# Optimization experiments

Hardware: AMD Instinct MI355X
Metric: run time of the kernel (lower is better)

## Reference

```python
import jax, jax.numpy as jnp
import numpy as np

EPS = 1e-12  # F.normalize eps


def _l2norm(v, axis):
    n = jnp.sqrt(jnp.sum(v * v, axis=axis, keepdims=True))
    return v / jnp.maximum(n, EPS)


def setup_inputs() -> dict:
    key = jax.random.key(0)
    k1, k2, k3, k4 = jax.random.split(key, 4)
    N, C, H, W = 48, 512, 40, 40
    K = 64
    x = jax.random.normal(k1, (N, C, H, W), dtype=jnp.float32)
    conv_w = jax.random.normal(k2, (K, C), dtype=jnp.float32) * 0.02   # cluster-assign 1x1 conv, no bias (vladv2=False)
    attn_w = jax.random.normal(k3, (1, C), dtype=jnp.float32) * 0.02   # heatmap 1x1 conv
    attn_b = jnp.zeros((1,), dtype=jnp.float32)
    centroids = jax.random.uniform(k4, (K, C), dtype=jnp.float32)      # torch.rand init
    return {"x": x, "conv_w": conv_w, "attn_w": attn_w, "attn_b": attn_b, "centroids": centroids}


def reference(x, conv_w, attn_w, attn_b, centroids):
    N, C, H, W = x.shape
    K = conv_w.shape[0]
    P = H * W

    # attention heatmap: ReLU -> 1x1 conv -> ReLU  => [N, 1, H, W]
    hmp = jax.nn.relu(jnp.einsum('nchw,oc->nohw', jax.nn.relu(x), attn_w) + attn_b[None, :, None, None])
    hmp_flat = hmp.reshape(N, 1, P)  # [N,1,P]

    # normalize input descriptors across channels
    xn = _l2norm(x, axis=1)                      # [N,C,H,W]
    x_flat = xn.reshape(N, C, P)                 # [N,C,P]

    # soft assignment: 1x1 conv over clusters + softmax over cluster dim
    logits = jnp.einsum('ncp,kc->nkp', x_flat, conv_w)   # [N,K,P]
    soft_assign = jax.nn.softmax(logits, axis=1)          # softmax over K

    # weighted residual aggregation, fused:
    # vlad[n,k,c] = sum_p (x[n,c,p] - centroids[k,c]) * sa[n,k,p] * hmp[n,0,p]
    w = soft_assign * hmp_flat                            # [N,K,P]
    term1 = jnp.einsum('nkp,ncp->nkc', w, x_flat)         # [N,K,C]
    wsum = jnp.sum(w, axis=-1)                            # [N,K]
    vlad = term1 - wsum[:, :, None] * centroids[None, :, :]

    vlad = _l2norm(vlad, axis=2)                          # intra-normalize per cluster
    vlad = vlad.reshape(N, K * C)
    vlad = _l2norm(vlad, axis=1)                          # global L2 normalize
    return vlad
```

## Files before the change

kernel.cpp:

```cpp
#include <hip/hip_runtime.h>
#include <math.h>

#define NN 48
#define CC 512
#define KK 64
#define PP 1600
#define EPSF 1e-12f

typedef short short8 __attribute__((ext_vector_type(8)));
typedef float f32x4 __attribute__((ext_vector_type(4)));

static __device__ __forceinline__ unsigned short f2bf(float f) {
    unsigned u = __float_as_uint(f);
    u += 0x7fffu + ((u >> 16) & 1u);
    return (unsigned short)(u >> 16);
}
static __device__ __forceinline__ unsigned pack2(float a, float b) {
    return (unsigned)f2bf(a) | ((unsigned)f2bf(b) << 16);
}

static __device__ __forceinline__ void barrier_nd() {
    asm volatile("s_waitcnt lgkmcnt(0)\n\ts_barrier" ::: "memory");
}

__global__ __launch_bounds__(256, 4) void kn_logits(
    const float* __restrict__ x, const float* __restrict__ conv_w,
    const float* __restrict__ attn_w, const float* __restrict__ attn_b,
    unsigned short* __restrict__ wg, float* __restrict__ wsum,
    unsigned short* __restrict__ xbf)
{
    __shared__ unsigned short xt[64][76];
    __shared__ unsigned short cwb[64][72];
    __shared__ float attn_l[CC];
    __shared__ float red[16][64];
    __shared__ float invn_l[64];
    __shared__ float hmp_l[64];
    __shared__ float wsum_l[KK];

    const int n = blockIdx.y, p0 = blockIdx.x * 64, tid = threadIdx.x;
    const int q = tid & 15, cg = tid >> 4;
    const int wave = tid >> 6, lane = tid & 63;
    const int lq = lane >> 4, lm = lane & 15;
    const int kr = tid >> 2, cq = tid & 3;

    for (int i = tid; i < CC; i += 256) attn_l[i] = attn_w[i];
    if (tid < KK) wsum_l[tid] = 0.f;

    f32x4 acc[4];
#pragma unroll
    for (int mt = 0; mt < 4; ++mt) acc[mt] = (f32x4){0.f, 0.f, 0.f, 0.f};
    float ss[4] = {0.f, 0.f, 0.f, 0.f};
    float ad[4] = {0.f, 0.f, 0.f, 0.f};

    const float* xb = x + (size_t)n * CC * PP;
    const float* wp0 = conv_w + (size_t)kr * CC + cq * 16;
    const float* xp0 = xb + (size_t)(cg * 4) * PP + p0 + 4 * q;

    float4 wv[4], xv[4];
#pragma unroll
    for (int j = 0; j < 4; ++j) wv[j] = *(const float4*)(wp0 + 4 * j);
#pragma unroll
    for (int j = 0; j < 4; ++j) xv[j] = *(const float4*)(xp0 + (size_t)j * PP);

    __syncthreads();

#pragma unroll 1
    for (int cs = 0; cs < 8; ++cs) {
        float4 wn[4], xn_[4];
        if (cs < 7) {
            const float* wp = wp0 + (cs + 1) * 64;
            const float* xp = xp0 + (size_t)(cs + 1) * 64 * PP;
#pragma unroll
            for (int j = 0; j < 4; ++j) wn[j] = *(const float4*)(wp + 4 * j);
#pragma unroll
            for (int j = 0; j < 4; ++j) xn_[j] = *(const float4*)(xp + (size_t)j * PP);
        }
#pragma unroll
        for (int j = 0; j < 4; ++j) {
            uint2 u = {pack2(wv[j].x, wv[j].y), pack2(wv[j].z, wv[j].w)};
            *(uint2*)&cwb[kr][cq * 16 + 4 * j] = u;
        }
        const int cbase = cs * 64 + cg * 4;
#pragma unroll
        for (int j = 0; j < 4; ++j) {
            float4 v = xv[j];
            const float aw = attn_l[cbase + j];
            ss[0] += v.x * v.x; ss[1] += v.y * v.y;
            ss[2] += v.z * v.z; ss[3] += v.w * v.w;
            ad[0] += fmaxf(v.x, 0.f) * aw; ad[1] += fmaxf(v.y, 0.f) * aw;
            ad[2] += fmaxf(v.z, 0.f) * aw; ad[3] += fmaxf(v.w, 0.f) * aw;
            uint2 u = {pack2(v.x, v.y), pack2(v.z, v.w)};
            *(uint2*)&xt[cg * 4 + j][4 * q] = u;
            if (xbf)
                *(uint2*)(xbf + ((size_t)n * CC + cbase + j) * PP + p0 + 4 * q) = u;
        }
        barrier_nd();
#pragma unroll
        for (int ks = 0; ks < 2; ++ks) {
            short8 af[4];
#pragma unroll
            for (int mt = 0; mt < 4; ++mt)
                af[mt] = *(const short8*)&cwb[mt * 16 + lm][ks * 32 + lq * 8];
            const int pl = wave * 16 + lm;
            const int cb = ks * 32 + lq * 8;
            short8 bv;
#pragma unroll
            for (int j = 0; j < 8; ++j) bv[j] = (short)xt[cb + j][pl];
#pragma unroll
            for (int mt = 0; mt < 4; ++mt)
                acc[mt] = __builtin_amdgcn_mfma_f32_16x16x32_bf16(
                    af[mt], bv, acc[mt], 0, 0, 0);
        }
        barrier_nd();
        if (cs < 7) {
#pragma unroll
            for (int j = 0; j < 4; ++j) { wv[j] = wn[j]; xv[j] = xn_[j]; }
        }
    }

#pragma unroll
    for (int j = 0; j < 4; ++j) red[cg][4 * q + j] = ss[j];
    __syncthreads();
    if (tid < 64) {
        float S = 0.f;
#pragma unroll
        for (int l = 0; l < 16; ++l) S += red[l][tid];
        invn_l[tid] = 1.f / fmaxf(sqrtf(S), EPSF);
    }
    __syncthreads();
#pragma unroll
    for (int j = 0; j < 4; ++j) red[cg][4 * q + j] = ad[j];
    __syncthreads();
    if (tid < 64) {
        float A = 0.f;
#pragma unroll
        for (int l = 0; l < 16; ++l) A += red[l][tid];
        hmp_l[tid] = fmaxf(A + attn_b[0], 0.f);
    }
    __syncthreads();

    const int pl = wave * 16 + lm;
    const float inv = invn_l[pl];
    const float hp = hmp_l[pl];
    float mx = -1e30f;
#pragma unroll
    for (int mt = 0; mt < 4; ++mt)
#pragma unroll
        for (int r = 0; r < 4; ++r) {
            const float l = acc[mt][r] * inv;
            acc[mt][r] = l;
            mx = fmaxf(mx, l);
        }
    mx = fmaxf(mx, __shfl_xor(mx, 16));
    mx = fmaxf(mx, __shfl_xor(mx, 32));
    float s = 0.f;
#pragma unroll
    for (int mt = 0; mt < 4; ++mt)
#pragma unroll
        for (int r = 0; r < 4; ++r) {
            const float e = __expf(acc[mt][r] - mx);
            acc[mt][r] = e;
            s += e;
        }
    s += __shfl_xor(s, 16);
    s += __shfl_xor(s, 32);
    const float sden = hp / s;

    unsigned short* wrb = wg + (size_t)n * KK * PP + p0;
#pragma unroll
    for (int mt = 0; mt < 4; ++mt)
#pragma unroll
        for (int r = 0; r < 4; ++r) {
            const int k = mt * 16 + lq * 4 + r;
            const float w0 = acc[mt][r] * sden;
            float wk = w0;
#pragma unroll
            for (int o = 1; o < 16; o <<= 1) wk += __shfl_xor(wk, o);
            if (lm == 0) atomicAdd(&wsum_l[k], wk);
            wrb[(size_t)k * PP + pl] = f2bf(w0 * inv);
        }
    __syncthreads();
    if (tid < KK) atomicAdd(&wsum[n * KK + tid], wsum_l[tid]);
}

template <bool XB>
__global__ __launch_bounds__(256) void kn_term1(
    const float* __restrict__ xf, const unsigned short* __restrict__ xbf,
    const unsigned short* __restrict__ wgq, float* __restrict__ term1p)
{
    __shared__ unsigned short wt[64][40];
    __shared__ unsigned short xt2[64][40];
    const int c0 = blockIdx.x * 64, n = blockIdx.y, ph = blockIdx.z;
    const int tid = threadIdx.x;
    const int wave = tid >> 6, lane = tid & 63, lq = lane >> 4, lm = lane & 15;
    const int koff = (wave >> 1) * 32, coff = (wave & 1) * 32;
    const int s_begin = (50 * ph) >> 2, s_end = (50 * (ph + 1)) >> 2;
    const int rA = tid >> 2, cq = tid & 3;

    f32x4 acc[2][2];
#pragma unroll
    for (int mt = 0; mt < 2; ++mt)
#pragma unroll
        for (int nt = 0; nt < 2; ++nt) acc[mt][nt] = (f32x4){0.f, 0.f, 0.f, 0.f};

    const unsigned short* wb = wgq + (size_t)n * KK * PP + (size_t)rA * PP + cq * 8;
    const unsigned short* xbb = xbf + ((size_t)n * CC + c0 + rA) * PP + cq * 8;
    const float* xfb = xf + ((size_t)n * CC + c0 + rA) * PP + cq * 8;

    auto ldB = [&](int p) -> uint4 {
        if (XB) {
            return *(const uint4*)(xbb + p);
        } else {
            const float* sp = xfb + p;
            float4 a = *(const float4*)sp, b = *(const float4*)(sp + 4);
            return make_uint4(pack2(a.x, a.y), pack2(a.z, a.w),
                              pack2(b.x, b.y), pack2(b.z, b.w));
        }
    };

    uint4 pa = *(const uint4*)(wb + s_begin * 32);
    uint4 pb = ldB(s_begin * 32);

    for (int ps = s_begin; ps < s_end; ++ps) {
        uint4 na, nb;
        if (ps + 1 < s_end) {
            na = *(const uint4*)(wb + (ps + 1) * 32);
            nb = ldB((ps + 1) * 32);
        }
        *(uint4*)&wt[rA][cq * 8] = pa;
        *(uint4*)&xt2[rA][cq * 8] = pb;
        barrier_nd();
        short8 af[2], bv[2];
#pragma unroll
        for (int mt = 0; mt < 2; ++mt)
            af[mt] = *(const short8*)&wt[koff + mt * 16 + lm][lq * 8];
#pragma unroll
        for (int nt = 0; nt < 2; ++nt)
            bv[nt] = *(const short8*)&xt2[coff + nt * 16 + lm][lq * 8];
#pragma unroll
        for (int mt = 0; mt < 2; ++mt)
#pragma unroll
            for (int nt = 0; nt < 2; ++nt)
                acc[mt][nt] = __builtin_amdgcn_mfma_f32_16x16x32_bf16(
                    af[mt], bv[nt], acc[mt][nt], 0, 0, 0);
        barrier_nd();
        pa = na; pb = nb;
    }

    float* ob = term1p + ((size_t)ph * NN + n) * KK * CC + c0 + coff;
#pragma unroll
    for (int mt = 0; mt < 2; ++mt)
#pragma unroll
        for (int r = 0; r < 4; ++r) {
            const int k = koff + mt * 16 + lq * 4 + r;
#pragma unroll
            for (int nt = 0; nt < 2; ++nt)
                ob[(size_t)k * CC + nt * 16 + lm] = acc[mt][nt][r];
        }
}

__global__ __launch_bounds__(128) void kn_vlad(
    const float* __restrict__ term1p, const float* __restrict__ wsum,
    const float* __restrict__ cent, float* __restrict__ out,
    float* __restrict__ nsum)
{
    const int k = blockIdx.x, n = blockIdx.y, tid = threadIdx.x;
    const size_t base = ((size_t)n * KK + k) * CC;
    const size_t NKC = (size_t)NN * KK * CC;
    const float ws = wsum[n * KK + k];
    const int c = tid * 4;

    float4 ce = *(const float4*)(cent + (size_t)k * CC + c);
    float4 v = {-ws * ce.x, -ws * ce.y, -ws * ce.z, -ws * ce.w};
#pragma unroll
    for (int h = 0; h < 4; ++h) {
        float4 a = *(const float4*)(term1p + h * NKC + base + c);
        v.x += a.x; v.y += a.y; v.z += a.z; v.w += a.w;
    }

    float s = v.x * v.x + v.y * v.y + v.z * v.z + v.w * v.w;
#pragma unroll
    for (int o = 32; o >= 1; o >>= 1) s += __shfl_down(s, o, 64);

    __shared__ float rb[2];
    __shared__ float sinv;
    if ((tid & 63) == 0) rb[tid >> 6] = s;
    __syncthreads();
    if (tid == 0) {
        const float S = rb[0] + rb[1];
        const float inv = 1.f / fmaxf(sqrtf(S), EPSF);
        sinv = inv;
        atomicAdd(&nsum[n], S * inv * inv);
    }
    __syncthreads();
    const float inv = sinv;
    float4 o4 = {v.x * inv, v.y * inv, v.z * inv, v.w * inv};
    *(float4*)(out + base + c) = o4;
}

__global__ __launch_bounds__(256) void kn_scale(
    float* __restrict__ out, const float* __restrict__ nsum)
{
    const int n = blockIdx.y;
    const size_t off = ((size_t)blockIdx.x * 256 + threadIdx.x) * 4;
    const float g = 1.f / fmaxf(sqrtf(nsum[n]), EPSF);
    float4 v = *(float4*)(out + (size_t)n * KK * CC + off);
    v.x *= g; v.y *= g; v.z *= g; v.w *= g;
    *(float4*)(out + (size_t)n * KK * CC + off) = v;
}

extern "C" void kernel_launch(void* const* d_in, const int* in_sizes, int n_in,
                              void* d_out, int out_size, void* d_ws, size_t ws_size,
                              hipStream_t stream)
{
    (void)in_sizes; (void)n_in; (void)out_size;
    const float* x      = (const float*)d_in[0];
    const float* conv_w = (const float*)d_in[1];
    const float* attn_w = (const float*)d_in[2];
    const float* attn_b = (const float*)d_in[3];
    const float* cent   = (const float*)d_in[4];
    float* out = (float*)d_out;

    char* w = (char*)d_ws;
    float* term1p = (float*)w;            w += (size_t)4 * NN * KK * CC * 4;
    float* wsum   = (float*)w;            w += (size_t)NN * KK * 4;
    float* nsum   = (float*)w;            w += 256;
    unsigned short* wg  = (unsigned short*)w; w += (size_t)NN * KK * PP * 2;
    unsigned short* xbf = (unsigned short*)w;
    const size_t need_xb = (size_t)(w - (char*)d_ws) + (size_t)NN * CC * PP * 2;
    const bool xb = ws_size >= need_xb;

    hipMemsetAsync(wsum, 0, NN * KK * sizeof(float), stream);
    hipMemsetAsync(nsum, 0, NN * sizeof(float), stream);

    kn_logits<<<dim3(25, NN), 256, 0, stream>>>(x, conv_w, attn_w, attn_b,
                                                wg, wsum, xb ? xbf : nullptr);
    if (xb)
        kn_term1<true><<<dim3(8, NN, 4), 256, 0, stream>>>(x, xbf, wg, term1p);
    else
        kn_term1<false><<<dim3(8, NN, 4), 256, 0, stream>>>(x, xbf, wg, term1p);
    kn_vlad <<<dim3(KK, NN), 128, 0, stream>>>(term1p, wsum, cent, out, nsum);
    kn_scale<<<dim3(32, NN), 256, 0, stream>>>(out, nsum);
}
```

Baseline: 324.1 us.

## Use direct global-to-LDS DMA with double buffering in logits and term1 kernels

Both the logits and term1 kernels now load input tiles with global_load_lds straight into double-buffered, XOR-swizzled shared memory. The next chunk's copy is issued before the current one is computed. Register staging goes away and the bf16 conversion in logits now happens on read from LDS. The aim is to hide global memory latency and cut VGPR pressure. In exchange, the fp32 tile doubles LDS use, the occupancy hint drops from 4 to 3 blocks, and correctness now depends on hand-written vmcnt waits.

```diff
diff --git a/kernel.cpp b/kernel.cpp
--- a/kernel.cpp
+++ b/kernel.cpp
@@ -23,19 +23,21 @@
     asm volatile("s_waitcnt lgkmcnt(0)\n\ts_barrier" ::: "memory");
 }
 
-__global__ __launch_bounds__(256, 4) void kn_logits(
+typedef __attribute__((address_space(3))) unsigned int as3_uint;
+typedef __attribute__((address_space(1))) const unsigned int as1_cuint;
+static __device__ __forceinline__ void dma16(const void* g, void* l) {
+    __builtin_amdgcn_global_load_lds((as1_cuint*)g, (as3_uint*)l, 16, 0, 0);
+}
+
+__global__ __launch_bounds__(256, 3) void kn_logits(
     const float* __restrict__ x, const float* __restrict__ conv_w,
     const float* __restrict__ attn_w, const float* __restrict__ attn_b,
     unsigned short* __restrict__ wg, float* __restrict__ wsum,
     unsigned short* __restrict__ xbf)
 {
-    __shared__ unsigned short xt[64][76];
+    __shared__ float xf[2][64][64];
     __shared__ unsigned short cwb[64][72];
     __shared__ float attn_l[CC];
-    __shared__ float red[16][64];
-    __shared__ float invn_l[64];
-    __shared__ float hmp_l[64];
-    __shared__ float wsum_l[KK];
 
     const int n = blockIdx.y, p0 = blockIdx.x * 64, tid = threadIdx.x;
     const int q = tid & 15, cg = tid >> 4;
@@ -43,8 +45,27 @@
     const int lq = lane >> 4, lm = lane & 15;
     const int kr = tid >> 2, cq = tid & 3;
 
+    const float* xb = x + (size_t)n * CC * PP;
+    const int dsub = lane >> 4, dslot = lane & 15;
+
+    auto dma_chunk = [&](int cs, int nb) {
+#pragma unroll
+        for (int i = 0; i < 4; ++i) {
+            const int row = (i * 4 + wave) * 4 + dsub;
+            const int qlog = dslot ^ (row & 7);
+            const float* g = xb + (size_t)(cs * 64 + row) * PP + p0 + qlog * 4;
+            dma16((const void*)g, (void*)&xf[nb][row][dslot * 4]);
+        }
+    };
+
+    dma_chunk(0, 0);
+
     for (int i = tid; i < CC; i += 256) attn_l[i] = attn_w[i];
-    if (tid < KK) wsum_l[tid] = 0.f;
+
+    float4 wv[4];
+    const float* wp0 = conv_w + (size_t)kr * CC + cq * 16;
+#pragma unroll
+    for (int j = 0; j < 4; ++j) wv[j] = *(const float4*)(wp0 + 4 * j);
 
     f32x4 acc[4];
 #pragma unroll
@@ -52,89 +73,93 @@
     float ss[4] = {0.f, 0.f, 0.f, 0.f};
     float ad[4] = {0.f, 0.f, 0.f, 0.f};
 
-    const float* xb = x + (size_t)n * CC * PP;
-    const float* wp0 = conv_w + (size_t)kr * CC + cq * 16;
-    const float* xp0 = xb + (size_t)(cg * 4) * PP + p0 + 4 * q;
-
-    float4 wv[4], xv[4];
-#pragma unroll
-    for (int j = 0; j < 4; ++j) wv[j] = *(const float4*)(wp0 + 4 * j);
-#pragma unroll
-    for (int j = 0; j < 4; ++j) xv[j] = *(const float4*)(xp0 + (size_t)j * PP);
-
-    __syncthreads();
-
 #pragma unroll 1
     for (int cs = 0; cs < 8; ++cs) {
-        float4 wn[4], xn_[4];
-        if (cs < 7) {
-            const float* wp = wp0 + (cs + 1) * 64;
-            const float* xp = xp0 + (size_t)(cs + 1) * 64 * PP;
-#pragma unroll
-            for (int j = 0; j < 4; ++j) wn[j] = *(const float4*)(wp + 4 * j);
-#pragma unroll
-            for (int j = 0; j < 4; ++j) xn_[j] = *(const float4*)(xp + (size_t)j * PP);
-        }
+        const int b = cs & 1;
+        barrier_nd();
+        const int csn = cs < 7 ? cs + 1 : 7;
+        dma_chunk(csn, b ^ 1);
 #pragma unroll
         for (int j = 0; j < 4; ++j) {
             uint2 u = {pack2(wv[j].x, wv[j].y), pack2(wv[j].z, wv[j].w)};
             *(uint2*)&cwb[kr][cq * 16 + 4 * j] = u;
         }
+        float4 wn[4];
+        if (cs < 7) {
+            const float* wp = wp0 + (cs + 1) * 64;
+#pragma unroll
+            for (int j = 0; j < 4; ++j) wn[j] = *(const float4*)(wp + 4 * j);
+        }
+        __builtin_amdgcn_sched_barrier(0);
+        asm volatile("s_waitcnt vmcnt(4)" ::: "memory");
+        __builtin_amdgcn_sched_barrier(0);
+        barrier_nd();
+
         const int cbase = cs * 64 + cg * 4;
 #pragma unroll
         for (int j = 0; j < 4; ++j) {
-            float4 v = xv[j];
+            const int row = cg * 4 + j;
+            const float4 v = *(const float4*)&xf[b][row][(q ^ (row & 7)) * 4];
             const float aw = attn_l[cbase + j];
             ss[0] += v.x * v.x; ss[1] += v.y * v.y;
             ss[2] += v.z * v.z; ss[3] += v.w * v.w;
             ad[0] += fmaxf(v.x, 0.f) * aw; ad[1] += fmaxf(v.y, 0.f) * aw;
             ad[2] += fmaxf(v.z, 0.f) * aw; ad[3] += fmaxf(v.w, 0.f) * aw;
             uint2 u = {pack2(v.x, v.y), pack2(v.z, v.w)};
-            *(uint2*)&xt[cg * 4 + j][4 * q] = u;
             if (xbf)
                 *(uint2*)(xbf + ((size_t)n * CC + cbase + j) * PP + p0 + 4 * q) = u;
         }
-        barrier_nd();
+        const int pl = wave * 16 + lm;
 #pragma unroll
         for (int ks = 0; ks < 2; ++ks) {
             short8 af[4];
 #pragma unroll
             for (int mt = 0; mt < 4; ++mt)
                 af[mt] = *(const short8*)&cwb[mt * 16 + lm][ks * 32 + lq * 8];
-            const int pl = wave * 16 + lm;
             const int cb = ks * 32 + lq * 8;
             short8 bv;
 #pragma unroll
-            for (int j = 0; j < 8; ++j) bv[j] = (short)xt[cb + j][pl];
+            for (int jj = 0; jj < 8; ++jj) {
+                const int row = cb + jj;
+                const float xv = xf[b][row][(((pl >> 2) ^ (row & 7)) << 2) + (pl & 3)];
+                bv[jj] = (short)f2bf(xv);
+            }
 #pragma unroll
             for (int mt = 0; mt < 4; ++mt)
                 acc[mt] = __builtin_amdgcn_mfma_f32_16x16x32_bf16(
                     af[mt], bv, acc[mt], 0, 0, 0);
         }
-        barrier_nd();
         if (cs < 7) {
 #pragma unroll
-            for (int j = 0; j < 4; ++j) { wv[j] = wn[j]; xv[j] = xn_[j]; }
-        }
-    }
-
-#pragma unroll
-    for (int j = 0; j < 4; ++j) red[cg][4 * q + j] = ss[j];
+            for (int j = 0; j < 4; ++j) wv[j] = wn[j];
+        }
+    }
+
+    __syncthreads();
+
+    float* red    = &xf[0][0][0];
+    float* invn_l = &xf[1][0][0];
+    float* hmp_l  = invn_l + 64;
+    float* wsum_l = invn_l + 128;
+
+    if (tid < KK) wsum_l[tid] = 0.f;
+#pragma unroll
+    for (int j = 0; j < 4; ++j) red[cg * 64 + 4 * q + j] = ss[j];
     __syncthreads();
     if (tid < 64) {
         float S = 0.f;
 #pragma unroll
-        for (int l = 0; l < 16; ++l) S += red[l][tid];
+        for (int l = 0; l < 16; ++l) S += red[l * 64 + tid];
         invn_l[tid] = 1.f / fmaxf(sqrtf(S), EPSF);
     }
     __syncthreads();
 #pragma unroll
-    for (int j = 0; j < 4; ++j) red[cg][4 * q + j] = ad[j];
+    for (int j = 0; j < 4; ++j) red[cg * 64 + 4 * q + j] = ad[j];
     __syncthreads();
     if (tid < 64) {
         float A = 0.f;
 #pragma unroll
-        for (int l = 0; l < 16; ++l) A += red[l][tid];
+        for (int l = 0; l < 16; ++l) A += red[l * 64 + tid];
         hmp_l[tid] = fmaxf(A + attn_b[0], 0.f);
     }
     __syncthreads();
@@ -183,10 +208,84 @@
     if (tid < KK) atomicAdd(&wsum[n * KK + tid], wsum_l[tid]);
 }
 
-template <bool XB>
-__global__ __launch_bounds__(256) void kn_term1(
-    const float* __restrict__ xf, const unsigned short* __restrict__ xbf,
+__global__ __launch_bounds__(256) void kn_term1_dma(
+    const unsigned short* __restrict__ xbf,
     const unsigned short* __restrict__ wgq, float* __restrict__ term1p)
+{
+    __shared__ unsigned short wt[2][64][32];
+    __shared__ unsigned short xt2[2][64][32];
+    const int c0 = blockIdx.x * 64, n = blockIdx.y, ph = blockIdx.z;
+    const int tid = threadIdx.x;
+    const int wave = tid >> 6, lane = tid & 63, lq = lane >> 4, lm = lane & 15;
+    const int koff = (wave >> 1) * 32, coff = (wave & 1) * 32;
+    const int s_begin = (50 * ph) >> 2, s_end = (50 * (ph + 1)) >> 2;
+
+    const int drow = wave * 16 + (lane >> 2);
+    const int dslot = lane & 3;
+    const int dq = dslot ^ (drow & 3);
+
+    const unsigned short* wsrc = wgq + (size_t)n * KK * PP + (size_t)drow * PP + dq * 8;
+    const unsigned short* xsrc = xbf + ((size_t)n * CC + c0 + drow) * PP + dq * 8;
+
+    auto dma_tiles = [&](int ps, int nb) {
+        dma16((const void*)(wsrc + ps * 32), (void*)&wt[nb][drow][dslot * 8]);
+        dma16((const void*)(xsrc + ps * 32), (void*)&xt2[nb][drow][dslot * 8]);
+    };
+
+    f32x4 acc[2][2];
+#pragma unroll
+    for (int mt = 0; mt < 2; ++mt)
+#pragma unroll
+        for (int nt = 0; nt < 2; ++nt) acc[mt][nt] = (f32x4){0.f, 0.f, 0.f, 0.f};
+
+    dma_tiles(s_begin, 0);
+
+#pragma unroll 1
+    for (int ps = s_begin; ps < s_end; ++ps) {
+        const int b = (ps - s_begin) & 1;
+        barrier_nd();
+        const int psn = (ps + 1 < s_end) ? ps + 1 : ps;
+        dma_tiles(psn, b ^ 1);
+        __builtin_amdgcn_sched_barrier(0);
+        asm volatile("s_waitcnt vmcnt(2)" ::: "memory");
+        __builtin_amdgcn_sched_barrier(0);
+        barrier_nd();
+
+        short8 af[2], bv[2];
+#pragma unroll
+        for (int mt = 0; mt < 2; ++mt) {
+            const int row = koff + mt * 16 + lm;
+            af[mt] = *(const short8*)&wt[b][row][(lq ^ (row & 3)) * 8];
+        }
+#pragma unroll
+        for (int nt = 0; nt < 2; ++nt) {
+            const int row = coff + nt * 16 + lm;
+            bv[nt] = *(const short8*)&xt2[b][row][(lq ^ (row & 3)) * 8];
+        }
+#pragma unroll
+        for (int mt = 0; mt < 2; ++mt)
+#pragma unroll
+            for (int nt = 0; nt < 2; ++nt)
+                acc[mt][nt] = __builtin_amdgcn_mfma_f32_16x16x32_bf16(
+                    af[mt], bv[nt], acc[mt][nt], 0, 0, 0);
+    }
+    asm volatile("s_waitcnt vmcnt(0)" ::: "memory");
+
+    float* ob = term1p + ((size_t)ph * NN + n) * KK * CC + c0 + coff;
+#pragma unroll
+    for (int mt = 0; mt < 2; ++mt)
+#pragma unroll
+        for (int r = 0; r < 4; ++r) {
+            const int k = koff + mt * 16 + lq * 4 + r;
+#pragma unroll
+            for (int nt = 0; nt < 2; ++nt)
+                ob[(size_t)k * CC + nt * 16 + lm] = acc[mt][nt][r];
+        }
+}
+
+__global__ __launch_bounds__(256) void kn_term1_f32(
+    const float* __restrict__ xf, const unsigned short* __restrict__ wgq,
+    float* __restrict__ term1p)
 {
     __shared__ unsigned short wt[64][40];
     __shared__ unsigned short xt2[64][40];
@@ -204,18 +303,13 @@
         for (int nt = 0; nt < 2; ++nt) acc[mt][nt] = (f32x4){0.f, 0.f, 0.f, 0.f};
 
     const unsigned short* wb = wgq + (size_t)n * KK * PP + (size_t)rA * PP + cq * 8;
-    const unsigned short* xbb = xbf + ((size_t)n * CC + c0 + rA) * PP + cq * 8;
     const float* xfb = xf + ((size_t)n * CC + c0 + rA) * PP + cq * 8;
 
     auto ldB = [&](int p) -> uint4 {
-        if (XB) {
-            return *(const uint4*)(xbb + p);
-        } else {
-            const float* sp = xfb + p;
-            float4 a = *(const float4*)sp, b = *(const float4*)(sp + 4);
-            return make_uint4(pack2(a.x, a.y), pack2(a.z, a.w),
-                              pack2(b.x, b.y), pack2(b.z, b.w));
-        }
+        const float* sp = xfb + p;
+        float4 a = *(const float4*)sp, b = *(const float4*)(sp + 4);
+        return make_uint4(pack2(a.x, a.y), pack2(a.z, a.w),
+                          pack2(b.x, b.y), pack2(b.z, b.w));
     };
 
     uint4 pa = *(const uint4*)(wb + s_begin * 32);
@@ -229,7 +323,7 @@
         }
         *(uint4*)&wt[rA][cq * 8] = pa;
         *(uint4*)&xt2[rA][cq * 8] = pb;
-        barrier_nd();
+        __syncthreads();
         short8 af[2], bv[2];
 #pragma unroll
         for (int mt = 0; mt < 2; ++mt)
@@ -243,7 +337,7 @@
             for (int nt = 0; nt < 2; ++nt)
                 acc[mt][nt] = __builtin_amdgcn_mfma_f32_16x16x32_bf16(
                     af[mt], bv[nt], acc[mt][nt], 0, 0, 0);
-        barrier_nd();
+        __syncthreads();
         pa = na; pb = nb;
     }
 
@@ -336,9 +430,9 @@
     kn_logits<<<dim3(25, NN), 256, 0, stream>>>(x, conv_w, attn_w, attn_b,
                                                 wg, wsum, xb ? xbf : nullptr);
     if (xb)
-        kn_term1<true><<<dim3(8, NN, 4), 256, 0, stream>>>(x, xbf, wg, term1p);
+        kn_term1_dma<<<dim3(8, NN, 4), 256, 0, stream>>>(xbf, wg, term1p);
     else
-        kn_term1<false><<<dim3(8, NN, 4), 256, 0, stream>>>(x, xbf, wg, term1p);
+        kn_term1_f32<<<dim3(8, NN, 4), 256, 0, stream>>>(x, wg, term1p);
     kn_vlad <<<dim3(KK, NN), 128, 0, stream>>>(term1p, wsum, cent, out, nsum);
     kn_scale<<<dim3(32, NN), 256, 0, stream>>>(out, nsum);
 }
```

Result: no change. 318.6 us (-1.7%).
